# Performance work log

Measured on AMD Instinct MI355X. Metric: run time of the kernel, lower is better.

The kernel has to match this reference:

```python
import jax, jax.numpy as jnp
import numpy as np

D_MODEL, N_LAYER, VOCAB = 1024, 4, 50280
D_INNER, D_STATE, D_CONV, DT_RANK = 2048, 16, 4, 64
B, L = 1, 1024
EPS = 1e-5


def _rmsnorm(x, w):
    var = jnp.mean(jnp.square(x), axis=-1, keepdims=True)
    return x * jax.lax.rsqrt(var + EPS) * w


def _selective_scan(u, dt, A, Bm, Cm, Dv):
    # u, dt: [b,l,d]; A: [d,n]; Bm, Cm: [b,l,n]; Dv: [d]
    dA = jnp.exp(dt[..., None] * A)                      # [b,l,d,n]
    dBu = dt[..., None] * Bm[:, :, None, :] * u[..., None]  # [b,l,d,n]

    def step(s, x):
        dA_t, dBu_t, C_t = x
        s = s * dA_t + dBu_t                             # [b,d,n]
        y = jnp.einsum('bdn,bn->bd', s, C_t)
        return s, y

    s0 = jnp.zeros((u.shape[0], u.shape[2], A.shape[1]), u.dtype)
    xs = (dA.transpose(1, 0, 2, 3), dBu.transpose(1, 0, 2, 3), Cm.transpose(1, 0, 2))
    _, ys = jax.lax.scan(step, s0, xs)                   # ys: [l,b,d]
    return ys.transpose(1, 0, 2) + u * Dv


def _mixer(x, in_w, cw, cb, xp_w, dt_w, dt_b, A_log, Dv, out_w):
    Lx = x.shape[1]
    xz = jnp.einsum('bld,ed->ble', x, in_w)              # [b,l,2*d_inner]
    xp, z = jnp.split(xz, 2, axis=-1)
    # causal depthwise conv1d, kernel size D_CONV
    xpad = jnp.pad(xp, ((0, 0), (D_CONV - 1, 0), (0, 0)))
    conv = cb + sum(xpad[:, k:k + Lx, :] * cw[:, k] for k in range(D_CONV))
    u = jax.nn.silu(conv)
    xdbl = jnp.einsum('bld,ed->ble', u, xp_w)            # [b,l,dt_rank+2n]
    dt_r = xdbl[..., :DT_RANK]
    Bm = xdbl[..., DT_RANK:DT_RANK + D_STATE]
    Cm = xdbl[..., DT_RANK + D_STATE:]
    dt = jax.nn.softplus(jnp.einsum('blr,dr->bld', dt_r, dt_w) + dt_b)
    A = -jnp.exp(A_log)
    y = _selective_scan(u, dt, A, Bm, Cm, Dv)
    y = y * jax.nn.silu(z)
    return jnp.einsum('bld,ed->ble', y, out_w)


def _forward(input_ids, embedding, norm_w, in_proj_w, conv_w, conv_b, x_proj_w,
             dt_proj_w, dt_proj_b, A_log, D, out_proj_w, norm_f_w):
    hidden = embedding[input_ids]                        # [b,l,d_model]
    residual = None
    for i in range(N_LAYER):
        residual = hidden if residual is None else hidden + residual
        x = _rmsnorm(residual, norm_w[i])
        hidden = _mixer(x, in_proj_w[i], conv_w[i], conv_b[i], x_proj_w[i],
                        dt_proj_w[i], dt_proj_b[i], A_log[i], D[i], out_proj_w[i])
    residual = hidden + residual
    hf = _rmsnorm(residual, norm_f_w)
    # lm_head weight is tied to embedding
    return jnp.einsum('bld,vd->blv', hf, embedding)


def setup_inputs() -> dict:
    key = jax.random.key(0)
    ks = jax.random.split(key, 8)
    s = 0.02
    return {
        'input_ids': jax.random.randint(ks[0], (B, L), 0, VOCAB),
        'embedding': jax.random.normal(ks[1], (VOCAB, D_MODEL), jnp.float32) * s,
        'norm_w': jnp.ones((N_LAYER, D_MODEL), jnp.float32),
        'in_proj_w': jax.random.normal(ks[2], (N_LAYER, 2 * D_INNER, D_MODEL), jnp.float32) * s,
        'conv_w': jax.random.normal(ks[3], (N_LAYER, D_INNER, D_CONV), jnp.float32) * s,
        'conv_b': jnp.zeros((N_LAYER, D_INNER), jnp.float32),
        'x_proj_w': jax.random.normal(ks[4], (N_LAYER, DT_RANK + 2 * D_STATE, D_INNER), jnp.float32) * s,
        'dt_proj_w': jax.random.normal(ks[5], (N_LAYER, D_INNER, DT_RANK), jnp.float32) * s,
        'dt_proj_b': jnp.full((N_LAYER, D_INNER), -4.6, jnp.float32),  # softplus ~= 0.01
        'A_log': jnp.tile(jnp.log(jnp.arange(1.0, D_STATE + 1.0, dtype=jnp.float32))[None, None, :],
                          (N_LAYER, D_INNER, 1)),
        'D': jnp.ones((N_LAYER, D_INNER), jnp.float32),
        'out_proj_w': jax.random.normal(ks[6], (N_LAYER, D_MODEL, D_INNER), jnp.float32) * s,
        'norm_f_w': jnp.ones((D_MODEL,), jnp.float32),
    }


def reference(input_ids, embedding, norm_w, in_proj_w, conv_w, conv_b, x_proj_w,
              dt_proj_w, dt_proj_b, A_log, D, out_proj_w, norm_f_w):
    return _forward(input_ids, embedding, norm_w, in_proj_w, conv_w, conv_b,
                    x_proj_w, dt_proj_w, dt_proj_b, A_log, D, out_proj_w, norm_f_w)
```

## Files before the change

### kernel.cpp

```cpp
#include <hip/hip_runtime.h>
#include <hip/hip_bf16.h>

#define D_MODEL 1024
#define N_LAYER 4
#define D_INNER 2048
#define D_STATE 16
#define D_CONV  4
#define DT_RANK 64
#define SEQ_L   1024
#define VOCAB   50280
#define VOCAB_PAD 50304
#define NCHUNK  32
#define CLEN    32

typedef __attribute__((ext_vector_type(8))) short short8;
typedef __attribute__((ext_vector_type(4))) float f32x4;

typedef __attribute__((address_space(1))) const unsigned GUint;
typedef __attribute__((address_space(3))) unsigned LUint;

__device__ __forceinline__ float silu_f(float x) {
    return x / (1.0f + __expf(-x));
}
__device__ __forceinline__ float softplus_f(float x) {
    return fmaxf(x, 0.0f) + log1pf(__expf(-fabsf(x)));
}
__device__ __forceinline__ ushort f2bf(float f) {
    union { float f; unsigned u; } uf; uf.f = f;
    unsigned r = uf.u + 0x7FFF + ((uf.u >> 16) & 1);
    return (ushort)(r >> 16);
}

__global__ void f32_to_bf16_kernel(const float* __restrict__ in,
                                   ushort* __restrict__ out, int n4) {
    int i = blockIdx.x * 256 + threadIdx.x;
    if (i >= n4) return;
    float4 v = *(const float4*)(in + (size_t)i * 4);
    ushort4 o;
    o.x = f2bf(v.x); o.y = f2bf(v.y); o.z = f2bf(v.z); o.w = f2bf(v.w);
    *(ushort4*)(out + (size_t)i * 4) = o;
}

__global__ void xpw_convert_kernel(const float* __restrict__ src,
                                   ushort* __restrict__ dst) {
    int q = blockIdx.x * 256 + threadIdx.x;
    int layer = q / (128 * 512);
    int rq    = q % (128 * 512);
    int row   = rq / 512;
    int cq    = rq % 512;
    ushort4 o;
    if (row < 96) {
        float4 v = *(const float4*)(src + ((size_t)layer * 96 + row) * 2048 + cq * 4);
        o.x = f2bf(v.x); o.y = f2bf(v.y); o.z = f2bf(v.z); o.w = f2bf(v.w);
    } else {
        o.x = o.y = o.z = o.w = 0;
    }
    *(ushort4*)(dst + (size_t)q * 4) = o;
}

__global__ void embed_kernel(const int* __restrict__ ids,
                             const float* __restrict__ emb,
                             float* __restrict__ hidden) {
    int l = blockIdx.x;
    int t = threadIdx.x;
    int id = ids[l];
    float4 v = *(const float4*)(emb + (size_t)id * D_MODEL + t * 4);
    *(float4*)(hidden + (size_t)l * D_MODEL + t * 4) = v;
}

__global__ void add_rmsnorm_kernel(float* __restrict__ res,
                                   const float* __restrict__ part,
                                   const float* __restrict__ w,
                                   ushort* __restrict__ xout,
                                   int add, int nparts) {
    int l = blockIdx.x;
    int t = threadIdx.x;
    size_t base = (size_t)l * D_MODEL + t * 4;
    float4 r;
    if (add) r = *(const float4*)(res + base);
    else     r = make_float4(0.f, 0.f, 0.f, 0.f);
    for (int s = 0; s < nparts; ++s) {
        float4 hv = *(const float4*)(part + (size_t)s * SEQ_L * D_MODEL + base);
        r.x += hv.x; r.y += hv.y; r.z += hv.z; r.w += hv.w;
    }
    *(float4*)(res + base) = r;
    float ss = r.x * r.x + r.y * r.y + r.z * r.z + r.w * r.w;
    #pragma unroll
    for (int off = 32; off > 0; off >>= 1) ss += __shfl_down(ss, off, 64);
    __shared__ float sred[4];
    if ((t & 63) == 0) sred[t >> 6] = ss;
    __syncthreads();
    float tot = sred[0] + sred[1] + sred[2] + sred[3];
    float scale = rsqrtf(tot * (1.0f / (float)D_MODEL) + 1e-5f);
    float4 wv = *(const float4*)(w + t * 4);
    ushort4 o;
    o.x = f2bf(r.x * scale * wv.x);
    o.y = f2bf(r.y * scale * wv.y);
    o.z = f2bf(r.z * scale * wv.z);
    o.w = f2bf(r.w * scale * wv.w);
    *(ushort4*)(xout + base) = o;
}

template<int SPLIT>
__global__ void gemm_bf16_gld_kernel(const ushort* __restrict__ A,
                                     const ushort* __restrict__ W,
                                     float* __restrict__ C,
                                     int N, int K, int lda, int ldc,
                                     int MB, int KS, int pstride) {
    __shared__ ushort As[2][128][32];
    __shared__ ushort Ws[2][128][32];
    const int t  = threadIdx.x;
    const int T  = gridDim.x >> 3;
    const int id = blockIdx.x;
    const int j  = (id & 7) * T + (id >> 3);
    const int ks  = j % KS;
    const int rem = j / KS;
    const int m0 = (rem % MB) * 128;
    const int n0 = (rem / MB) * 128;
    const int kchunk = K / KS;
    const int kbeg = ks * kchunk;
    const int kend = kbeg + kchunk;

    const int lane = t & 63;
    const int w    = t >> 6;
    const int srow = w * 16 + (lane >> 2);
    const int scol = (((lane & 3) ^ ((lane >> 3) & 3)) * 8);
    const ushort* Ag0 = A + (size_t)(m0 + srow) * lda + scol;
    const ushort* Ag1 = A + (size_t)(m0 + srow + 64) * lda + scol;
    const ushort* Wg0 = W + (size_t)(n0 + srow) * K + scol;
    const ushort* Wg1 = W + (size_t)(n0 + srow + 64) * K + scol;

    const int wm = (t >> 7) & 1;
    const int wn = (t >> 6) & 1;
    const int lr = lane & 15;
    const int lk = lane >> 4;
    const int swz = (lr >> 1) & 3;

    f32x4 acc[4][4] = {};

#define STAGE_GLD(buf, kk)                                                        \
    do {                                                                          \
        __builtin_amdgcn_global_load_lds((GUint*)(Ag0 + (kk)),                    \
            (LUint*)&As[buf][w * 16][0], 16, 0, 0);                               \
        __builtin_amdgcn_global_load_lds((GUint*)(Ag1 + (kk)),                    \
            (LUint*)&As[buf][64 + w * 16][0], 16, 0, 0);                          \
        __builtin_amdgcn_global_load_lds((GUint*)(Wg0 + (kk)),                    \
            (LUint*)&Ws[buf][w * 16][0], 16, 0, 0);                               \
        __builtin_amdgcn_global_load_lds((GUint*)(Wg1 + (kk)),                    \
            (LUint*)&Ws[buf][64 + w * 16][0], 16, 0, 0);                          \
    } while (0)

    STAGE_GLD(0, kbeg);
    int buf = 0;
    for (int k0 = kbeg;;) {
        __syncthreads();
        const bool more = (k0 + 32) < kend;
        if (more) STAGE_GLD(buf ^ 1, k0 + 32);

        short8 af[4], bfr[4];
        #pragma unroll
        for (int m = 0; m < 4; ++m)
            af[m] = *(const short8*)&As[buf][wm * 64 + m * 16 + lr][(lk ^ swz) * 8];
        #pragma unroll
        for (int n = 0; n < 4; ++n)
            bfr[n] = *(const short8*)&Ws[buf][wn * 64 + n * 16 + lr][(lk ^ swz) * 8];
        #pragma unroll
        for (int m = 0; m < 4; ++m)
            #pragma unroll
            for (int n = 0; n < 4; ++n)
                acc[m][n] = __builtin_amdgcn_mfma_f32_16x16x32_bf16(
                    af[m], bfr[n], acc[m][n], 0, 0, 0);

        if (!more) break;
        buf ^= 1;
        k0 += 32;
    }
#undef STAGE_GLD

    float* Cp = SPLIT ? (C + (size_t)ks * pstride) : C;
    #pragma unroll
    for (int m = 0; m < 4; ++m) {
        const int row = m0 + wm * 64 + m * 16 + lk * 4;
        #pragma unroll
        for (int n = 0; n < 4; ++n) {
            const int col = n0 + wn * 64 + n * 16 + lr;
            if (col < N) {
                #pragma unroll
                for (int r = 0; r < 4; ++r)
                    Cp[(size_t)(row + r) * ldc + col] = acc[m][n][r];
            }
        }
    }
}

__global__ void xdbl_reduce_kernel(const float* __restrict__ part,
                                   float* __restrict__ out) {
    int i = blockIdx.x * 256 + threadIdx.x;
    float4 acc = make_float4(0.f, 0.f, 0.f, 0.f);
    #pragma unroll
    for (int s = 0; s < 16; ++s) {
        float4 v = *(const float4*)(part + (size_t)s * SEQ_L * 96 + (size_t)i * 4);
        acc.x += v.x; acc.y += v.y; acc.z += v.z; acc.w += v.w;
    }
    *(float4*)(out + (size_t)i * 4) = acc;
}

template<int EPI>
__global__ void gemm_tn_kernel(const float* __restrict__ A,
                               const float* __restrict__ W,
                               const float* __restrict__ bias,
                               float* __restrict__ C,
                               int M, int N, int K, int lda) {
    __shared__ float As[16][68];
    __shared__ float Ws[16][68];
    const int t  = threadIdx.x;
    const int m0 = blockIdx.y * 64;
    const int n0 = blockIdx.x * 64;
    const int lrow = t >> 2;
    const int lkq  = (t & 3) * 4;
    const int tx = t & 15;
    const int ty = t >> 4;

    const float* Arow = A + (size_t)(m0 + lrow) * lda;
    const int   wr    = n0 + lrow;
    const bool  wvalid = wr < N;
    const float* Wrow = W + (size_t)(wvalid ? wr : 0) * K;

    float acc[4][4] = {};
    for (int k0 = 0; k0 < K; k0 += 16) {
        float4 av = *(const float4*)(Arow + k0 + lkq);
        float4 wv = wvalid ? *(const float4*)(Wrow + k0 + lkq)
                           : make_float4(0.f, 0.f, 0.f, 0.f);
        As[lkq + 0][lrow] = av.x; As[lkq + 1][lrow] = av.y;
        As[lkq + 2][lrow] = av.z; As[lkq + 3][lrow] = av.w;
        Ws[lkq + 0][lrow] = wv.x; Ws[lkq + 1][lrow] = wv.y;
        Ws[lkq + 2][lrow] = wv.z; Ws[lkq + 3][lrow] = wv.w;
        __syncthreads();
        #pragma unroll
        for (int kk = 0; kk < 16; ++kk) {
            float4 a = *(const float4*)&As[kk][ty * 4];
            float4 b = *(const float4*)&Ws[kk][tx * 4];
            #pragma unroll
            for (int i = 0; i < 4; ++i) {
                float ai = (i == 0) ? a.x : (i == 1) ? a.y : (i == 2) ? a.z : a.w;
                acc[i][0] = fmaf(ai, b.x, acc[i][0]);
                acc[i][1] = fmaf(ai, b.y, acc[i][1]);
                acc[i][2] = fmaf(ai, b.z, acc[i][2]);
                acc[i][3] = fmaf(ai, b.w, acc[i][3]);
            }
        }
        __syncthreads();
    }

    const int colb = n0 + tx * 4;
    if (colb < N) {
        #pragma unroll
        for (int i = 0; i < 4; ++i) {
            int row = m0 + ty * 4 + i;
            float4 v = make_float4(acc[i][0], acc[i][1], acc[i][2], acc[i][3]);
            if (EPI == 1) {
                v.x = softplus_f(v.x + bias[colb + 0]);
                v.y = softplus_f(v.y + bias[colb + 1]);
                v.z = softplus_f(v.z + bias[colb + 2]);
                v.w = softplus_f(v.w + bias[colb + 3]);
            }
            *(float4*)(C + (size_t)row * N + colb) = v;
        }
    }
}

__global__ void conv_silu_kernel(const float* __restrict__ xz,
                                 const float* __restrict__ cw,
                                 const float* __restrict__ cb,
                                 float* __restrict__ u,
                                 ushort* __restrict__ u_b) {
    int idx = blockIdx.x * 256 + threadIdx.x;
    int l = idx >> 11;
    int c = idx & 2047;
    float acc = cb[c];
    float w0 = cw[c * 4 + 0], w1 = cw[c * 4 + 1], w2 = cw[c * 4 + 2], w3 = cw[c * 4 + 3];
    if (l >= 3) acc = fmaf(xz[(size_t)(l - 3) * 4096 + c], w0, acc);
    if (l >= 2) acc = fmaf(xz[(size_t)(l - 2) * 4096 + c], w1, acc);
    if (l >= 1) acc = fmaf(xz[(size_t)(l - 1) * 4096 + c], w2, acc);
    acc = fmaf(xz[(size_t)l * 4096 + c], w3, acc);
    float s = silu_f(acc);
    u[idx] = s;
    u_b[idx] = f2bf(s);
}

__global__ void scan_a_kernel(const float* __restrict__ u,
                              const float* __restrict__ dt,
                              const float* __restrict__ xdbl,
                              const float* __restrict__ A_log,
                              float* __restrict__ yloc,
                              float* __restrict__ cumdt,
                              float* __restrict__ s_end) {
    const int idx = blockIdx.x * 256 + threadIdx.x;
    const int d = idx & 2047;
    const int c = idx >> 11;

    float Aa[16];
    #pragma unroll
    for (int q = 0; q < 4; ++q) {
        float4 al = *(const float4*)(A_log + (size_t)d * 16 + q * 4);
        Aa[q * 4 + 0] = -__expf(al.x);
        Aa[q * 4 + 1] = -__expf(al.y);
        Aa[q * 4 + 2] = -__expf(al.z);
        Aa[q * 4 + 3] = -__expf(al.w);
    }

    float s[16];
    #pragma unroll
    for (int n = 0; n < 16; ++n) s[n] = 0.0f;
    float cd = 0.0f;

    const int l0 = c * CLEN;
    for (int i = 0; i < CLEN; ++i) {
        const int l = l0 + i;
        const float dtl = dt[(size_t)l * 2048 + d];
        const float ul  = u[(size_t)l * 2048 + d];
        float Bn[16], Cn[16];
        const float* xbp = xdbl + (size_t)l * 96;
        *(float4*)&Bn[0]  = *(const float4*)(xbp + 64);
        *(float4*)&Bn[4]  = *(const float4*)(xbp + 68);
        *(float4*)&Bn[8]  = *(const float4*)(xbp + 72);
        *(float4*)&Bn[12] = *(const float4*)(xbp + 76);
        *(float4*)&Cn[0]  = *(const float4*)(xbp + 80);
        *(float4*)&Cn[4]  = *(const float4*)(xbp + 84);
        *(float4*)&Cn[8]  = *(const float4*)(xbp + 88);
        *(float4*)&Cn[12] = *(const float4*)(xbp + 92);
        cd += dtl;
        const float dtu = dtl * ul;
        float y = 0.0f;
        #pragma unroll
        for (int n = 0; n < 16; ++n) {
            float dA = __expf(dtl * Aa[n]);
            s[n] = fmaf(s[n], dA, dtu * Bn[n]);
            y = fmaf(s[n], Cn[n], y);
        }
        yloc[(size_t)l * 4096 + d] = y;
        cumdt[(size_t)l * 2048 + d] = cd;
    }
    float* se = s_end + ((size_t)d * NCHUNK + c) * 16;
    #pragma unroll
    for (int q = 0; q < 4; ++q)
        *(float4*)(se + q * 4) = make_float4(s[q * 4], s[q * 4 + 1], s[q * 4 + 2], s[q * 4 + 3]);
}

__global__ void scan_b_kernel(const float* __restrict__ s_end,
                              const float* __restrict__ cumdt,
                              const float* __restrict__ A_log,
                              float* __restrict__ s_in) {
    const int idx = blockIdx.x * 256 + threadIdx.x;
    const int d = idx >> 4;
    const int n = idx & 15;
    const float Aa = -__expf(A_log[(size_t)d * 16 + n]);
    float s = 0.0f;
    #pragma unroll
    for (int c = 0; c < NCHUNK; ++c) {
        s_in[((size_t)d * NCHUNK + c) * 16 + n] = s;
        const float tot = cumdt[(size_t)(c * CLEN + CLEN - 1) * 2048 + d];
        s = s_end[((size_t)d * NCHUNK + c) * 16 + n] + __expf(Aa * tot) * s;
    }
}

__global__ void scan_c_kernel(const float* __restrict__ u,
                              const float* __restrict__ xdbl,
                              const float* __restrict__ A_log,
                              const float* __restrict__ Dv,
                              const float* __restrict__ xz,
                              const float* __restrict__ cumdt,
                              const float* __restrict__ s_in,
                              ushort* __restrict__ yb) {
    const int idx = blockIdx.x * 256 + threadIdx.x;
    const int l = idx >> 11;
    const int d = idx & 2047;
    const int c = l >> 5;

    const float cd = cumdt[idx];
    const float ul = u[idx];
    const float yv = xz[(size_t)l * 4096 + d];
    const float zv = xz[(size_t)l * 4096 + 2048 + d];
    const float* Cp = xdbl + (size_t)l * 96 + 80;
    const float* si = s_in + ((size_t)d * NCHUNK + c) * 16;

    float corr = 0.0f;
    #pragma unroll
    for (int q = 0; q < 4; ++q) {
        float4 al = *(const float4*)(A_log + (size_t)d * 16 + q * 4);
        float4 cv = *(const float4*)(Cp + q * 4);
        float4 sv = *(const float4*)(si + q * 4);
        corr = fmaf(cv.x * __expf(-__expf(al.x) * cd), sv.x, corr);
        corr = fmaf(cv.y * __expf(-__expf(al.y) * cd), sv.y, corr);
        corr = fmaf(cv.z * __expf(-__expf(al.z) * cd), sv.z, corr);
        corr = fmaf(cv.w * __expf(-__expf(al.w) * cd), sv.w, corr);
    }
    const float y = (yv + corr + Dv[d] * ul) * silu_f(zv);
    yb[idx] = f2bf(y);
}

extern "C" void kernel_launch(void* const* d_in, const int* in_sizes, int n_in,
                              void* d_out, int out_size, void* d_ws, size_t ws_size,
                              hipStream_t stream) {
    const int*   ids        = (const int*)d_in[0];
    const float* emb        = (const float*)d_in[1];
    const float* norm_w     = (const float*)d_in[2];
    const float* in_proj_w  = (const float*)d_in[3];
    const float* conv_w     = (const float*)d_in[4];
    const float* conv_b     = (const float*)d_in[5];
    const float* x_proj_w   = (const float*)d_in[6];
    const float* dt_proj_w  = (const float*)d_in[7];
    const float* dt_proj_b  = (const float*)d_in[8];
    const float* A_log      = (const float*)d_in[9];
    const float* Dv         = (const float*)d_in[10];
    const float* out_proj_w = (const float*)d_in[11];
    const float* norm_f_w   = (const float*)d_in[12];
    float* out = (float*)d_out;

    char* p = (char*)d_ws;
    ushort* emb_b  = (ushort*)p; p += (size_t)VOCAB_PAD * D_MODEL * 2;
    ushort* inw_b  = (ushort*)p; p += (size_t)N_LAYER * 4096 * 1024 * 2;
    ushort* outw_b = (ushort*)p; p += (size_t)N_LAYER * 1024 * 2048 * 2;
    ushort* xpw_b  = (ushort*)p; p += (size_t)N_LAYER * 128 * 2048 * 2;
    float* residual = (float*)p; p += (size_t)SEQ_L * D_MODEL * 4;
    float* hpart    = (float*)p; p += (size_t)4 * SEQ_L * D_MODEL * 4;
    float* xdpart   = (float*)p; p += (size_t)16 * SEQ_L * 96 * 4;
    float* xdbl     = (float*)p; p += (size_t)SEQ_L * 96 * 4;
    ushort* xb      = (ushort*)p; p += (size_t)SEQ_L * D_MODEL * 2;
    float* xz       = (float*)p; p += (size_t)SEQ_L * 4096 * 4;
    float* u        = (float*)p; p += (size_t)SEQ_L * 2048 * 4;
    ushort* u_b     = (ushort*)p; p += (size_t)SEQ_L * 2048 * 2;
    float* dtb      = (float*)p; p += (size_t)SEQ_L * 2048 * 4;
    ushort* yb      = (ushort*)p; p += (size_t)SEQ_L * 2048 * 2;
    float* cumdt    = (float*)p; p += (size_t)SEQ_L * 2048 * 4;
    float* s_end    = (float*)p; p += (size_t)D_INNER * NCHUNK * 16 * 4;
    float* s_in     = (float*)p; p += (size_t)D_INNER * NCHUNK * 16 * 4;

    dim3 blk(256);

    f32_to_bf16_kernel<<<dim3(VOCAB * D_MODEL / 4 / 256), blk, 0, stream>>>(
        emb, emb_b, VOCAB * D_MODEL / 4);
    f32_to_bf16_kernel<<<dim3(N_LAYER * 4096 * 1024 / 4 / 256), blk, 0, stream>>>(
        in_proj_w, inw_b, N_LAYER * 4096 * 1024 / 4);
    f32_to_bf16_kernel<<<dim3(N_LAYER * 1024 * 2048 / 4 / 256), blk, 0, stream>>>(
        out_proj_w, outw_b, N_LAYER * 1024 * 2048 / 4);
    xpw_convert_kernel<<<dim3(N_LAYER * 128 * 2048 / 4 / 256), blk, 0, stream>>>(
        x_proj_w, xpw_b);

    embed_kernel<<<dim3(SEQ_L), blk, 0, stream>>>(ids, emb, hpart);

    for (int i = 0; i < N_LAYER; ++i) {
        add_rmsnorm_kernel<<<dim3(SEQ_L), blk, 0, stream>>>(
            residual, hpart, norm_w + (size_t)i * D_MODEL, xb,
            i == 0 ? 0 : 1, i == 0 ? 1 : 4);

        gemm_bf16_gld_kernel<0><<<dim3(256), blk, 0, stream>>>(
            xb, inw_b + (size_t)i * 4096 * 1024, xz, 4096, 1024, 1024, 4096, 8, 1, 0);

        conv_silu_kernel<<<dim3(SEQ_L * D_INNER / 256), blk, 0, stream>>>(
            xz, conv_w + (size_t)i * D_INNER * D_CONV, conv_b + (size_t)i * D_INNER,
            u, u_b);

        gemm_bf16_gld_kernel<1><<<dim3(128), blk, 0, stream>>>(
            u_b, xpw_b + (size_t)i * 128 * 2048, xdpart, 96, 2048, 2048, 96,
            8, 16, SEQ_L * 96);
        xdbl_reduce_kernel<<<dim3(SEQ_L * 96 / 4 / 256), blk, 0, stream>>>(
            xdpart, xdbl);

        gemm_tn_kernel<1><<<dim3(D_INNER / 64, SEQ_L / 64), blk, 0, stream>>>(
            xdbl, dt_proj_w + (size_t)i * D_INNER * DT_RANK,
            dt_proj_b + (size_t)i * D_INNER, dtb,
            SEQ_L, D_INNER, DT_RANK, 96);

        scan_a_kernel<<<dim3(D_INNER * NCHUNK / 256), blk, 0, stream>>>(
            u, dtb, xdbl, A_log + (size_t)i * D_INNER * D_STATE, xz, cumdt, s_end);
        scan_b_kernel<<<dim3(D_INNER * 16 / 256), blk, 0, stream>>>(
            s_end, cumdt, A_log + (size_t)i * D_INNER * D_STATE, s_in);
        scan_c_kernel<<<dim3(SEQ_L * D_INNER / 256), blk, 0, stream>>>(
            u, xdbl, A_log + (size_t)i * D_INNER * D_STATE,
            Dv + (size_t)i * D_INNER, xz, cumdt, s_in, yb);

        gemm_bf16_gld_kernel<1><<<dim3(256), blk, 0, stream>>>(
            yb, outw_b + (size_t)i * 1024 * 2048, hpart, 1024, 2048, 2048, 1024,
            8, 4, SEQ_L * D_MODEL);
    }

    add_rmsnorm_kernel<<<dim3(SEQ_L), blk, 0, stream>>>(
        residual, hpart, norm_f_w, xb, 1, 4);

    gemm_bf16_gld_kernel<0><<<dim3(3144), blk, 0, stream>>>(
        xb, emb_b, out, VOCAB, 1024, 1024, VOCAB, 8, 1, 0);
}
```

Baseline: 801.4 us.

## Use split-K partials for projections and move dt_proj to bf16 MFMA GEMM

Raises split-K factors for in_proj (1→2), x_proj (16→32) and out_proj (4→8) so more blocks run on the GPU. The partial sums are folded into the consumers (conv, scan_a, scan_c, rmsnorm) rather than reduced separately. The fp32 SIMT dt_proj GEMM is replaced by the bf16 MFMA GEMM with split-K 2, and its bias plus softplus are applied inside scan_a. This adds extra partial-buffer traffic and redundant loads in the consumers, and trades some precision on dt.

Measured after the change: 839.1 us. 4.7% more time.

```diff
diff --git a/kernel.cpp b/kernel.cpp
--- a/kernel.cpp
+++ b/kernel.cpp
@@ -194,78 +194,22 @@
 }
 
 __global__ void xdbl_reduce_kernel(const float* __restrict__ part,
-                                   float* __restrict__ out) {
+                                   float* __restrict__ out,
+                                   ushort* __restrict__ dtr_b) {
     int i = blockIdx.x * 256 + threadIdx.x;
     float4 acc = make_float4(0.f, 0.f, 0.f, 0.f);
     #pragma unroll
-    for (int s = 0; s < 16; ++s) {
+    for (int s = 0; s < 32; ++s) {
         float4 v = *(const float4*)(part + (size_t)s * SEQ_L * 96 + (size_t)i * 4);
         acc.x += v.x; acc.y += v.y; acc.z += v.z; acc.w += v.w;
     }
     *(float4*)(out + (size_t)i * 4) = acc;
-}
-
-template<int EPI>
-__global__ void gemm_tn_kernel(const float* __restrict__ A,
-                               const float* __restrict__ W,
-                               const float* __restrict__ bias,
-                               float* __restrict__ C,
-                               int M, int N, int K, int lda) {
-    __shared__ float As[16][68];
-    __shared__ float Ws[16][68];
-    const int t  = threadIdx.x;
-    const int m0 = blockIdx.y * 64;
-    const int n0 = blockIdx.x * 64;
-    const int lrow = t >> 2;
-    const int lkq  = (t & 3) * 4;
-    const int tx = t & 15;
-    const int ty = t >> 4;
-
-    const float* Arow = A + (size_t)(m0 + lrow) * lda;
-    const int   wr    = n0 + lrow;
-    const bool  wvalid = wr < N;
-    const float* Wrow = W + (size_t)(wvalid ? wr : 0) * K;
-
-    float acc[4][4] = {};
-    for (int k0 = 0; k0 < K; k0 += 16) {
-        float4 av = *(const float4*)(Arow + k0 + lkq);
-        float4 wv = wvalid ? *(const float4*)(Wrow + k0 + lkq)
-                           : make_float4(0.f, 0.f, 0.f, 0.f);
-        As[lkq + 0][lrow] = av.x; As[lkq + 1][lrow] = av.y;
-        As[lkq + 2][lrow] = av.z; As[lkq + 3][lrow] = av.w;
-        Ws[lkq + 0][lrow] = wv.x; Ws[lkq + 1][lrow] = wv.y;
-        Ws[lkq + 2][lrow] = wv.z; Ws[lkq + 3][lrow] = wv.w;
-        __syncthreads();
-        #pragma unroll
-        for (int kk = 0; kk < 16; ++kk) {
-            float4 a = *(const float4*)&As[kk][ty * 4];
-            float4 b = *(const float4*)&Ws[kk][tx * 4];
-            #pragma unroll
-            for (int i = 0; i < 4; ++i) {
-                float ai = (i == 0) ? a.x : (i == 1) ? a.y : (i == 2) ? a.z : a.w;
-                acc[i][0] = fmaf(ai, b.x, acc[i][0]);
-                acc[i][1] = fmaf(ai, b.y, acc[i][1]);
-                acc[i][2] = fmaf(ai, b.z, acc[i][2]);
-                acc[i][3] = fmaf(ai, b.w, acc[i][3]);
-            }
-        }
-        __syncthreads();
-    }
-
-    const int colb = n0 + tx * 4;
-    if (colb < N) {
-        #pragma unroll
-        for (int i = 0; i < 4; ++i) {
-            int row = m0 + ty * 4 + i;
-            float4 v = make_float4(acc[i][0], acc[i][1], acc[i][2], acc[i][3]);
-            if (EPI == 1) {
-                v.x = softplus_f(v.x + bias[colb + 0]);
-                v.y = softplus_f(v.y + bias[colb + 1]);
-                v.z = softplus_f(v.z + bias[colb + 2]);
-                v.w = softplus_f(v.w + bias[colb + 3]);
-            }
-            *(float4*)(C + (size_t)row * N + colb) = v;
-        }
+    int c = (i * 4) % 96;
+    if (c < 64) {
+        int r = (i * 4) / 96;
+        ushort4 o;
+        o.x = f2bf(acc.x); o.y = f2bf(acc.y); o.z = f2bf(acc.z); o.w = f2bf(acc.w);
+        *(ushort4*)(dtr_b + (size_t)r * 64 + c) = o;
     }
 }
 
@@ -279,17 +223,20 @@
     int c = idx & 2047;
     float acc = cb[c];
     float w0 = cw[c * 4 + 0], w1 = cw[c * 4 + 1], w2 = cw[c * 4 + 2], w3 = cw[c * 4 + 3];
-    if (l >= 3) acc = fmaf(xz[(size_t)(l - 3) * 4096 + c], w0, acc);
-    if (l >= 2) acc = fmaf(xz[(size_t)(l - 2) * 4096 + c], w1, acc);
-    if (l >= 1) acc = fmaf(xz[(size_t)(l - 1) * 4096 + c], w2, acc);
-    acc = fmaf(xz[(size_t)l * 4096 + c], w3, acc);
+#define XP(ll) (xz[(size_t)(ll) * 4096 + c] + xz[(size_t)SEQ_L * 4096 + (size_t)(ll) * 4096 + c])
+    if (l >= 3) acc = fmaf(XP(l - 3), w0, acc);
+    if (l >= 2) acc = fmaf(XP(l - 2), w1, acc);
+    if (l >= 1) acc = fmaf(XP(l - 1), w2, acc);
+    acc = fmaf(XP(l), w3, acc);
+#undef XP
     float s = silu_f(acc);
     u[idx] = s;
     u_b[idx] = f2bf(s);
 }
 
 __global__ void scan_a_kernel(const float* __restrict__ u,
-                              const float* __restrict__ dt,
+                              const float* __restrict__ dtp,
+                              const float* __restrict__ dt_bias,
                               const float* __restrict__ xdbl,
                               const float* __restrict__ A_log,
                               float* __restrict__ yloc,
@@ -308,6 +255,7 @@
         Aa[q * 4 + 2] = -__expf(al.z);
         Aa[q * 4 + 3] = -__expf(al.w);
     }
+    const float dbias = dt_bias[d];
 
     float s[16];
     #pragma unroll
@@ -317,7 +265,9 @@
     const int l0 = c * CLEN;
     for (int i = 0; i < CLEN; ++i) {
         const int l = l0 + i;
-        const float dtl = dt[(size_t)l * 2048 + d];
+        const float dtl = softplus_f(dtp[(size_t)l * 2048 + d]
+                                   + dtp[(size_t)SEQ_L * 2048 + (size_t)l * 2048 + d]
+                                   + dbias);
         const float ul  = u[(size_t)l * 2048 + d];
         float Bn[16], Cn[16];
         const float* xbp = xdbl + (size_t)l * 96;
@@ -380,7 +330,8 @@
     const float cd = cumdt[idx];
     const float ul = u[idx];
     const float yv = xz[(size_t)l * 4096 + d];
-    const float zv = xz[(size_t)l * 4096 + 2048 + d];
+    const float zv = xz[(size_t)l * 4096 + 2048 + d]
+                   + xz[(size_t)SEQ_L * 4096 + (size_t)l * 4096 + 2048 + d];
     const float* Cp = xdbl + (size_t)l * 96 + 80;
     const float* si = s_in + ((size_t)d * NCHUNK + c) * 16;
 
@@ -422,15 +373,16 @@
     ushort* inw_b  = (ushort*)p; p += (size_t)N_LAYER * 4096 * 1024 * 2;
     ushort* outw_b = (ushort*)p; p += (size_t)N_LAYER * 1024 * 2048 * 2;
     ushort* xpw_b  = (ushort*)p; p += (size_t)N_LAYER * 128 * 2048 * 2;
+    ushort* dtw_b  = (ushort*)p; p += (size_t)N_LAYER * 2048 * 64 * 2;
     float* residual = (float*)p; p += (size_t)SEQ_L * D_MODEL * 4;
-    float* hpart    = (float*)p; p += (size_t)4 * SEQ_L * D_MODEL * 4;
-    float* xdpart   = (float*)p; p += (size_t)16 * SEQ_L * 96 * 4;
+    float* hpart    = (float*)p; p += (size_t)8 * SEQ_L * D_MODEL * 4;
+    float* scratch  = (float*)p; p += (size_t)2 * SEQ_L * 2048 * 4;
     float* xdbl     = (float*)p; p += (size_t)SEQ_L * 96 * 4;
+    ushort* dtr_b   = (ushort*)p; p += (size_t)SEQ_L * 64 * 2;
     ushort* xb      = (ushort*)p; p += (size_t)SEQ_L * D_MODEL * 2;
-    float* xz       = (float*)p; p += (size_t)SEQ_L * 4096 * 4;
+    float* xzp      = (float*)p; p += (size_t)2 * SEQ_L * 4096 * 4;
     float* u        = (float*)p; p += (size_t)SEQ_L * 2048 * 4;
     ushort* u_b     = (ushort*)p; p += (size_t)SEQ_L * 2048 * 2;
-    float* dtb      = (float*)p; p += (size_t)SEQ_L * 2048 * 4;
     ushort* yb      = (ushort*)p; p += (size_t)SEQ_L * 2048 * 2;
     float* cumdt    = (float*)p; p += (size_t)SEQ_L * 2048 * 4;
     float* s_end    = (float*)p; p += (size_t)D_INNER * NCHUNK * 16 * 4;
@@ -444,6 +396,8 @@
         in_proj_w, inw_b, N_LAYER * 4096 * 1024 / 4);
     f32_to_bf16_kernel<<<dim3(N_LAYER * 1024 * 2048 / 4 / 256), blk, 0, stream>>>(
         out_proj_w, outw_b, N_LAYER * 1024 * 2048 / 4);
+    f32_to_bf16_kernel<<<dim3(N_LAYER * 2048 * 64 / 4 / 256), blk, 0, stream>>>(
+        dt_proj_w, dtw_b, N_LAYER * 2048 * 64 / 4);
     xpw_convert_kernel<<<dim3(N_LAYER * 128 * 2048 / 4 / 256), blk, 0, stream>>>(
         x_proj_w, xpw_b);
 
@@ -452,41 +406,42 @@
     for (int i = 0; i < N_LAYER; ++i) {
         add_rmsnorm_kernel<<<dim3(SEQ_L), blk, 0, stream>>>(
             residual, hpart, norm_w + (size_t)i * D_MODEL, xb,
-            i == 0 ? 0 : 1, i == 0 ? 1 : 4);
-
-        gemm_bf16_gld_kernel<0><<<dim3(256), blk, 0, stream>>>(
-            xb, inw_b + (size_t)i * 4096 * 1024, xz, 4096, 1024, 1024, 4096, 8, 1, 0);
+            i == 0 ? 0 : 1, i == 0 ? 1 : 8);
+
+        gemm_bf16_gld_kernel<1><<<dim3(512), blk, 0, stream>>>(
+            xb, inw_b + (size_t)i * 4096 * 1024, xzp, 4096, 1024, 1024, 4096,
+            8, 2, SEQ_L * 4096);
 
         conv_silu_kernel<<<dim3(SEQ_L * D_INNER / 256), blk, 0, stream>>>(
-            xz, conv_w + (size_t)i * D_INNER * D_CONV, conv_b + (size_t)i * D_INNER,
+            xzp, conv_w + (size_t)i * D_INNER * D_CONV, conv_b + (size_t)i * D_INNER,
             u, u_b);
 
-        gemm_bf16_gld_kernel<1><<<dim3(128), blk, 0, stream>>>(
-            u_b, xpw_b + (size_t)i * 128 * 2048, xdpart, 96, 2048, 2048, 96,
-            8, 16, SEQ_L * 96);
+        gemm_bf16_gld_kernel<1><<<dim3(256), blk, 0, stream>>>(
+            u_b, xpw_b + (size_t)i * 128 * 2048, scratch, 96, 2048, 2048, 96,
+            8, 32, SEQ_L * 96);
         xdbl_reduce_kernel<<<dim3(SEQ_L * 96 / 4 / 256), blk, 0, stream>>>(
-            xdpart, xdbl);
-
-        gemm_tn_kernel<1><<<dim3(D_INNER / 64, SEQ_L / 64), blk, 0, stream>>>(
-            xdbl, dt_proj_w + (size_t)i * D_INNER * DT_RANK,
-            dt_proj_b + (size_t)i * D_INNER, dtb,
-            SEQ_L, D_INNER, DT_RANK, 96);
+            scratch, xdbl, dtr_b);
+
+        gemm_bf16_gld_kernel<1><<<dim3(256), blk, 0, stream>>>(
+            dtr_b, dtw_b + (size_t)i * 2048 * 64, scratch, 2048, 64, 64, 2048,
+            8, 2, SEQ_L * 2048);
 
         scan_a_kernel<<<dim3(D_INNER * NCHUNK / 256), blk, 0, stream>>>(
-            u, dtb, xdbl, A_log + (size_t)i * D_INNER * D_STATE, xz, cumdt, s_end);
+            u, scratch, dt_proj_b + (size_t)i * D_INNER, xdbl,
+            A_log + (size_t)i * D_INNER * D_STATE, xzp, cumdt, s_end);
         scan_b_kernel<<<dim3(D_INNER * 16 / 256), blk, 0, stream>>>(
             s_end, cumdt, A_log + (size_t)i * D_INNER * D_STATE, s_in);
         scan_c_kernel<<<dim3(SEQ_L * D_INNER / 256), blk, 0, stream>>>(
             u, xdbl, A_log + (size_t)i * D_INNER * D_STATE,
-            Dv + (size_t)i * D_INNER, xz, cumdt, s_in, yb);
-
-        gemm_bf16_gld_kernel<1><<<dim3(256), blk, 0, stream>>>(
+            Dv + (size_t)i * D_INNER, xzp, cumdt, s_in, yb);
+
+        gemm_bf16_gld_kernel<1><<<dim3(512), blk, 0, stream>>>(
             yb, outw_b + (size_t)i * 1024 * 2048, hpart, 1024, 2048, 2048, 1024,
-            8, 4, SEQ_L * D_MODEL);
+            8, 8, SEQ_L * D_MODEL);
     }
 
     add_rmsnorm_kernel<<<dim3(SEQ_L), blk, 0, stream>>>(
-        residual, hpart, norm_f_w, xb, 1, 4);
+        residual, hpart, norm_f_w, xb, 1, 8);
 
     gemm_bf16_gld_kernel<0><<<dim3(3144), blk, 0, stream>>>(
         xb, emb_b, out, VOCAB, 1024, 1024, VOCAB, 8, 1, 0);
```

## Use 256x256 tile, 8-wave, multi-buffered bf16 GEMM for vocab LM head

Applied to the files above, without the earlier changes.

Adds a new LM-head GEMM kernel with 256x256 output tiles, 512 threads (8 waves), a 4-slot LDS ring with prefetch two tiles ahead via global_load_lds, swizzled LDS reads, and XCD-aware block remapping. The final vocab projection switches from the 128x128 generic kernel (3144 blocks) to this kernel (788 blocks). VOCAB_PAD grows to a multiple of 256 so the padded embedding covers full tiles. It aims for more data reuse per loaded tile and better overlap of loads with MFMA, at the cost of high register and LDS use per block and fewer, larger blocks that may leave some CUs idle.

After: 835.1 us. +4.2%, slower.

```diff
diff --git a/kernel.cpp b/kernel.cpp
--- a/kernel.cpp
+++ b/kernel.cpp
@@ -9,7 +9,7 @@
 #define DT_RANK 64
 #define SEQ_L   1024
 #define VOCAB   50280
-#define VOCAB_PAD 50304
+#define VOCAB_PAD 50432
 #define NCHUNK  32
 #define CLEN    32
 
@@ -193,6 +193,115 @@
     }
 }
 
+__global__ __launch_bounds__(512)
+void gemm_bf16_8ph_kernel(const ushort* __restrict__ A,
+                          const ushort* __restrict__ W,
+                          float* __restrict__ C,
+                          int N, int K, int lda, int ldc, int MB) {
+    __shared__ ushort As[4][256][32];
+    __shared__ ushort Bs[4][256][32];
+    const int t    = threadIdx.x;
+    const int lane = t & 63;
+    const int w    = t >> 6;
+
+    const int nwg = gridDim.x;
+    const int q = nwg >> 3, r = nwg & 7;
+    const int xcd = blockIdx.x & 7, pos = blockIdx.x >> 3;
+    const int j = (xcd < r ? xcd * (q + 1) : r * (q + 1) + (xcd - r) * q) + pos;
+    const int m0 = (j % MB) * 256;
+    const int n0 = (j / MB) * 256;
+
+    const int srow = (w << 4) + (lane >> 2);
+    const int scol = (((lane & 3) ^ ((lane >> 3) & 3)) << 3);
+    const ushort* Ag = A + (size_t)(m0 + srow) * lda + scol;
+    const ushort* Wg = W + (size_t)(n0 + srow) * K + scol;
+
+    const int wm = w >> 2;
+    const int wn = w & 3;
+    const int lr = lane & 15;
+    const int lk = lane >> 4;
+    const int rsw = ((lk ^ ((lr >> 1) & 3)) << 3);
+
+    f32x4 acc[8][4] = {};
+    const int NT = K >> 5;
+
+#define STG_A(buf, half, kk)                                                     \
+    __builtin_amdgcn_global_load_lds(                                           \
+        (GUint*)(Ag + (size_t)(half) * 128 * lda + (kk)),                        \
+        (LUint*)&As[buf][(half) * 128 + (w << 4)][0], 16, 0, 0)
+#define STG_B(buf, half, kk)                                                     \
+    __builtin_amdgcn_global_load_lds(                                           \
+        (GUint*)(Wg + (size_t)(half) * 128 * K + (kk)),                          \
+        (LUint*)&Bs[buf][(half) * 128 + (w << 4)][0], 16, 0, 0)
+
+    STG_A(0, 0, 0);  STG_A(0, 1, 0);  STG_B(0, 0, 0);  STG_B(0, 1, 0);
+    STG_A(1, 0, 32); STG_A(1, 1, 32); STG_B(1, 0, 32); STG_B(1, 1, 32);
+    asm volatile("s_waitcnt vmcnt(4)" ::: "memory");
+    __builtin_amdgcn_s_barrier();
+    __builtin_amdgcn_sched_barrier(0);
+
+    for (int tt = 0; tt < NT; ++tt) {
+        const int buf  = tt & 3;
+        const bool pf  = (tt + 2) < NT;
+        const int pbuf = (tt + 2) & 3;
+        const int pk   = (tt + 2) << 5;
+
+        short8 a[4], b[4];
+
+        if (pf) { STG_A(pbuf, 0, pk); STG_A(pbuf, 1, pk); }
+        #pragma unroll
+        for (int m = 0; m < 4; ++m)
+            a[m] = *(const short8*)&As[buf][wm * 128 + m * 16 + lr][rsw];
+        #pragma unroll
+        for (int n = 0; n < 4; ++n)
+            b[n] = *(const short8*)&Bs[buf][wn * 64 + n * 16 + lr][rsw];
+        __builtin_amdgcn_s_setprio(1);
+        #pragma unroll
+        for (int m = 0; m < 4; ++m)
+            #pragma unroll
+            for (int n = 0; n < 4; ++n)
+                acc[m][n] = __builtin_amdgcn_mfma_f32_16x16x32_bf16(
+                    a[m], b[n], acc[m][n], 0, 0, 0);
+        __builtin_amdgcn_s_setprio(0);
+
+        if (pf) { STG_B(pbuf, 0, pk); STG_B(pbuf, 1, pk); }
+        #pragma unroll
+        for (int m = 0; m < 4; ++m)
+            a[m] = *(const short8*)&As[buf][wm * 128 + (m + 4) * 16 + lr][rsw];
+        __builtin_amdgcn_s_setprio(1);
+        #pragma unroll
+        for (int m = 0; m < 4; ++m)
+            #pragma unroll
+            for (int n = 0; n < 4; ++n)
+                acc[m + 4][n] = __builtin_amdgcn_mfma_f32_16x16x32_bf16(
+                    a[m], b[n], acc[m + 4][n], 0, 0, 0);
+        __builtin_amdgcn_s_setprio(0);
+
+        if (tt + 1 < NT) {
+            if (pf) asm volatile("s_waitcnt vmcnt(4)" ::: "memory");
+            else    asm volatile("s_waitcnt vmcnt(0)" ::: "memory");
+            __builtin_amdgcn_s_barrier();
+            __builtin_amdgcn_sched_barrier(0);
+        }
+    }
+#undef STG_A
+#undef STG_B
+
+    #pragma unroll
+    for (int m = 0; m < 8; ++m) {
+        const int row = m0 + wm * 128 + m * 16 + lk * 4;
+        #pragma unroll
+        for (int n = 0; n < 4; ++n) {
+            const int col = n0 + wn * 64 + n * 16 + lr;
+            if (col < N) {
+                #pragma unroll
+                for (int rr = 0; rr < 4; ++rr)
+                    C[(size_t)(row + rr) * ldc + col] = acc[m][n][rr];
+            }
+        }
+    }
+}
+
 __global__ void xdbl_reduce_kernel(const float* __restrict__ part,
                                    float* __restrict__ out) {
     int i = blockIdx.x * 256 + threadIdx.x;
@@ -488,6 +597,6 @@
     add_rmsnorm_kernel<<<dim3(SEQ_L), blk, 0, stream>>>(
         residual, hpart, norm_f_w, xb, 1, 4);
 
-    gemm_bf16_gld_kernel<0><<<dim3(3144), blk, 0, stream>>>(
-        xb, emb_b, out, VOCAB, 1024, 1024, VOCAB, 8, 1, 0);
-}
+    gemm_bf16_8ph_kernel<<<dim3(788), dim3(512), 0, stream>>>(
+        xb, emb_b, out, VOCAB, 1024, 1024, VOCAB, 4);
+}
```
